# Kernel tuning notes

Measured on AMD Instinct MI355X. Metric: run time of the kernel, lower is better.

## Reference

```python
import jax, jax.numpy as jnp
import numpy as np

B, T = 2, 1024
V, D, H, L = 32000, 1024, 16, 8
DH = D // H  # 64
ROPE_BASE = 1000.0
EPS = 1e-6


def _rms_norm(x):
    # F.rms_norm(x, (C,), eps=1e-6)
    ms = jnp.mean(jnp.square(x), axis=-1, keepdims=True)
    return x * jax.lax.rsqrt(ms + EPS)


def _rope_tables(t_len):
    quarter = DH // 4
    inv_freq = jnp.concatenate([
        ROPE_BASE ** (-jnp.arange(quarter, dtype=jnp.float32) / quarter),
        jnp.zeros(quarter, dtype=jnp.float32),
    ])  # [DH/2]
    theta = jnp.arange(t_len, dtype=jnp.float32)[:, None] * inv_freq[None, :]  # [T, DH/2]
    return jnp.cos(theta), jnp.sin(theta)


def _apply_rope(x, cos, sin):
    # x: [B, H, T, DH]; cos/sin: [T, DH/2] broadcast to [1,1,T,DH/2]
    half = DH // 2
    x1, x2 = x[..., :half], x[..., half:]
    c = cos[None, None]
    s = sin[None, None]
    return jnp.concatenate([c * x1 - s * x2, s * x1 + c * x2], axis=-1).astype(x.dtype)


def setup_inputs() -> dict:
    key = jax.random.key(0)
    ks = jax.random.split(key, 7)
    s = 0.02
    return {
        "x_indices": jax.random.randint(ks[0], (B, T), 0, V, dtype=jnp.int32),
        "embedding": jax.random.normal(ks[1], (V, D), dtype=jnp.float32) * s,
        "Wqkv": jax.random.normal(ks[2], (L, 3 * D, D), dtype=jnp.float32) * s,
        "Wout": jax.random.normal(ks[3], (L, D, D), dtype=jnp.float32) * s,
        "W1": jax.random.normal(ks[4], (L, 4 * D, D), dtype=jnp.float32) * s,
        "W2": jax.random.normal(ks[5], (L, D, 4 * D), dtype=jnp.float32) * s,
        "lm_head": jax.random.normal(ks[6], (V, D), dtype=jnp.float32) * s,
    }


def reference(x_indices, embedding, Wqkv, Wout, W1, W2, lm_head):
    x = embedding[x_indices]  # [B, T, D]
    cos, sin = _rope_tables(T)
    causal = jnp.tril(jnp.ones((T, T), dtype=bool))  # [T, T]
    neg = jnp.finfo(x.dtype).min
    scale = 1.0 / np.sqrt(DH)

    for l in range(L):
        n = _rms_norm(x)
        qkv = jnp.einsum('btd,ed->bte', n, Wqkv[l])  # [B, T, 3D]
        qkv = qkv.reshape(B, T, 3, H, DH)
        q = jnp.transpose(qkv[:, :, 0], (0, 2, 1, 3))  # [B, H, T, DH]
        k = jnp.transpose(qkv[:, :, 1], (0, 2, 1, 3))
        v = jnp.transpose(qkv[:, :, 2], (0, 2, 1, 3))
        q = _apply_rope(q, cos, sin)
        k = _apply_rope(k, cos, sin)
        scores = jnp.einsum('bhqd,bhkd->bhqk', q, k) * scale
        scores = jnp.where(causal[None, None], scores, neg)
        attn = jax.nn.softmax(scores, axis=-1)
        ctx = jnp.einsum('bhqk,bhkd->bhqd', attn, v)
        ctx = jnp.transpose(ctx, (0, 2, 1, 3)).reshape(B, T, D)
        x = x + jnp.einsum('btd,ed->bte', ctx, Wout[l])
        n = _rms_norm(x)
        h = jnp.square(jax.nn.relu(jnp.einsum('btd,fd->btf', n, W1[l])))  # [B, T, 4D]
        x = x + jnp.einsum('btf,df->btd', h, W2[l])

    logits = jnp.einsum('btd,vd->btv', _rms_norm(x), lm_head)
    return logits.astype(jnp.float32)
```

## Files before the change

### kernel.cpp

```cpp
#include <hip/hip_runtime.h>
#include <hip/hip_bf16.h>
#include <cmath>
#include <cstdint>

#define B_  2
#define T_  1024
#define V_  32000
#define D_  1024
#define H_  16
#define L_  8
#define DH_ 64

typedef __attribute__((ext_vector_type(8))) short bf16x8;
typedef __attribute__((ext_vector_type(4))) float f32x4;

__device__ __forceinline__ ushort f2bf(float f) {
    union { float f; uint32_t u; } v; v.f = f;
    uint32_t r = v.u + 0x7FFFu + ((v.u >> 16) & 1u);
    return (ushort)(r >> 16);
}
__device__ __forceinline__ float bf2f(ushort u) {
    union { uint32_t u; float f; } v; v.u = ((uint32_t)u) << 16;
    return v.f;
}

__device__ __forceinline__ void async_copy16(const void* g, void* l) {
    __builtin_amdgcn_global_load_lds(
        (const __attribute__((address_space(1))) void*)g,
        (__attribute__((address_space(3))) void*)l, 16, 0, 0);
}

__global__ __launch_bounds__(256) void k_cast(const float4* __restrict__ in,
                                              ushort4* __restrict__ out, int n4) {
    for (int i = blockIdx.x * 256 + threadIdx.x; i < n4; i += gridDim.x * 256) {
        float4 v = in[i];
        out[i] = make_ushort4(f2bf(v.x), f2bf(v.y), f2bf(v.z), f2bf(v.w));
    }
}

__global__ void k_rope_tables(float* __restrict__ cosT, float* __restrict__ sinT) {
    int t = blockIdx.x;
    int i = threadIdx.x;
    float invf = (i < 16) ? powf(1000.0f, -(float)i / 16.0f) : 0.0f;
    float th = (float)t * invf;
    cosT[t * 32 + i] = cosf(th);
    sinT[t * 32 + i] = sinf(th);
}

__global__ __launch_bounds__(256) void k_gather(const int* __restrict__ idx,
                                                const float* __restrict__ emb,
                                                float* __restrict__ x,
                                                ushort* __restrict__ xb,
                                                float* __restrict__ ss) {
    int row = blockIdx.x;
    int id = idx[row];
    float4 v = ((const float4*)(emb + (size_t)id * D_))[threadIdx.x];
    ((float4*)(x + (size_t)row * D_))[threadIdx.x] = v;
    *(ushort4*)(xb + (size_t)row * D_ + threadIdx.x * 4) =
        make_ushort4(f2bf(v.x), f2bf(v.y), f2bf(v.z), f2bf(v.w));
    float s = v.x * v.x + v.y * v.y + v.z * v.z + v.w * v.w;
    #pragma unroll
    for (int off = 1; off < 64; off <<= 1) s += __shfl_xor(s, off);
    __shared__ float wsum[4];
    int lane = threadIdx.x & 63, wv = threadIdx.x >> 6;
    if (lane == 0) wsum[wv] = s;
    __syncthreads();
    if (threadIdx.x == 0) ss[row] = wsum[0] + wsum[1] + wsum[2] + wsum[3];
}

template<int BN, int EPI, bool OUTBF, bool CONVB, bool RSCALE, bool SSOUT>
__global__ __launch_bounds__(256, 2) void k_mfma_gemm(const ushort* __restrict__ A,
                                                      const void* __restrict__ Wp,
                                                      void* __restrict__ Cp,
                                                      const float* __restrict__ Res,
                                                      const float* __restrict__ cosT,
                                                      const float* __restrict__ sinT,
                                                      const float* __restrict__ ssIn,
                                                      float* __restrict__ ssOut,
                                                      ushort* __restrict__ xbOut,
                                                      int M, int N, int K) {
    constexpr int BM = 128;
    constexpr int MI = 4;
    constexpr int NI = BN / 32;
    constexpr bool DBUF = (BN <= 128);
    constexpr int NB = DBUF ? 2 : 1;
    __shared__ ushort As[NB][BM][64];
    __shared__ ushort Bs[NB][BN][64];
    const int tid = threadIdx.x;
    const int wid = tid >> 6, lane = tid & 63;
    const int wr = wid >> 1, wc = wid & 1;
    const int r16 = lane & 15, kc = lane >> 4;
    const int rx = (r16 & 7) << 4;
    const int srow8 = tid >> 3;
    const int sdcp = tid & 7;

    const int nwg = gridDim.x * gridDim.y;
    int orig = blockIdx.y * gridDim.x + blockIdx.x;
    int swz = (nwg & 7) ? orig : ((orig & 7) * (nwg >> 3) + (orig >> 3));
    const size_t bm = (size_t)(swz % gridDim.x) * BM;
    const size_t bn = (size_t)(swz / gridDim.x) * BN;

    auto stage = [&](int buf, int k0) {
        #pragma unroll
        for (int i = 0; i < 4; i++) {
            const int row = i * 32 + srow8;
            const ushort* g = A + (bm + row) * (size_t)K + k0 + ((sdcp ^ (row & 7)) * 8);
            async_copy16(g, (char*)As + buf * (BM * 128) + (i * 256 + tid) * 16);
        }
        if constexpr (!CONVB) {
            const ushort* Wb = (const ushort*)Wp;
            #pragma unroll
            for (int i = 0; i < BN / 32; i++) {
                const int row = i * 32 + srow8;
                const ushort* g = Wb + (bn + row) * (size_t)K + k0 + ((sdcp ^ (row & 7)) * 8);
                async_copy16(g, (char*)Bs + buf * (BN * 128) + (i * 256 + tid) * 16);
            }
        } else {
            const float* Wf = (const float*)Wp;
            #pragma unroll
            for (int i = 0; i < BN / 32; i++) {
                const int row = i * 32 + srow8;
                const float* src = Wf + (bn + row) * (size_t)K + k0 + sdcp * 8;
                float4 v0 = *(const float4*)(src);
                float4 v1 = *(const float4*)(src + 4);
                union { ushort u[8]; bf16x8 v; } tmp;
                tmp.u[0] = f2bf(v0.x); tmp.u[1] = f2bf(v0.y);
                tmp.u[2] = f2bf(v0.z); tmp.u[3] = f2bf(v0.w);
                tmp.u[4] = f2bf(v1.x); tmp.u[5] = f2bf(v1.y);
                tmp.u[6] = f2bf(v1.z); tmp.u[7] = f2bf(v1.w);
                *(bf16x8*)((char*)Bs + buf * (BN * 128) + row * 128 + ((sdcp ^ (row & 7)) << 4)) = tmp.v;
            }
        }
    };

    f32x4 acc[MI][NI];
    #pragma unroll
    for (int mi = 0; mi < MI; mi++)
        #pragma unroll
        for (int ni = 0; ni < NI; ni++) {
            f32x4 z = {0.f, 0.f, 0.f, 0.f};
            acc[mi][ni] = z;
        }

    auto compute = [&](int buf) {
        #pragma unroll
        for (int kk = 0; kk < 2; kk++) {
            bf16x8 af[MI], bfr[NI];
            #pragma unroll
            for (int mi = 0; mi < MI; mi++)
                af[mi] = *(const bf16x8*)((const char*)As + buf * (BM * 128) +
                                          (wr * 64 + mi * 16 + r16) * 128 +
                                          ((kk * 64 + kc * 16) ^ rx));
            #pragma unroll
            for (int ni = 0; ni < NI; ni++)
                bfr[ni] = *(const bf16x8*)((const char*)Bs + buf * (BN * 128) +
                                           (wc * (BN / 2) + ni * 16 + r16) * 128 +
                                           ((kk * 64 + kc * 16) ^ rx));
            #pragma unroll
            for (int mi = 0; mi < MI; mi++)
                #pragma unroll
                for (int ni = 0; ni < NI; ni++)
                    acc[mi][ni] = __builtin_amdgcn_mfma_f32_16x16x32_bf16(af[mi], bfr[ni],
                                                                          acc[mi][ni], 0, 0, 0);
        }
    };

    const int KSTEPS = K >> 6;
    if constexpr (DBUF) {
        stage(0, 0);
        __syncthreads();
        for (int step = 0; step < KSTEPS; ++step) {
            const int cur = step & 1;
            if (step + 1 < KSTEPS) stage(cur ^ 1, (step + 1) << 6);
            compute(cur);
            __syncthreads();
        }
    } else {
        for (int step = 0; step < KSTEPS; ++step) {
            stage(0, step << 6);
            __syncthreads();
            compute(0);
            __syncthreads();
        }
    }

    #pragma unroll
    for (int mi = 0; mi < MI; mi++) {
        #pragma unroll
        for (int j = 0; j < 4; j++) {
            const size_t row = bm + wr * 64 + mi * 16 + (lane >> 4) * 4 + j;
            if constexpr (RSCALE) {
                const float sc = rsqrtf(ssIn[row] * (1.0f / 1024.0f) + 1e-6f);
                #pragma unroll
                for (int ni = 0; ni < NI; ni++) acc[mi][ni][j] *= sc;
            }
            if constexpr (EPI == 3) {
                static_assert(BN == 128, "rope epilogue assumes BN=128");
                const int sec = (int)((bn + wc * 64) >> 10);
                if (sec < 2) {
                    const int t = (int)(row & (T_ - 1));
                    #pragma unroll
                    for (int np = 0; np < 2; np++) {
                        const int i1 = np * 16 + r16;
                        float c = cosT[t * 32 + i1], s = sinT[t * 32 + i1];
                        float x1 = acc[mi][np][j], x2 = acc[mi][np + 2][j];
                        acc[mi][np][j]     = c * x1 - s * x2;
                        acc[mi][np + 2][j] = s * x1 + c * x2;
                    }
                }
            }
            float ssq = 0.f;
            #pragma unroll
            for (int ni = 0; ni < NI; ni++) {
                const size_t col = bn + wc * (BN / 2) + ni * 16 + r16;
                float v = acc[mi][ni][j];
                if constexpr (EPI == 1) v += Res[row * N + col];
                if constexpr (EPI == 2) { v = fmaxf(v, 0.f); v *= v; }
                if constexpr (SSOUT) {
                    ssq += v * v;
                    xbOut[row * N + col] = f2bf(v);
                }
                if constexpr (OUTBF) {
                    ((ushort*)Cp)[row * N + col] = f2bf(v);
                } else if constexpr (EPI == 0) {
                    __builtin_nontemporal_store(v, (float*)Cp + row * N + col);
                } else {
                    ((float*)Cp)[row * N + col] = v;
                }
            }
            if constexpr (SSOUT) {
                #pragma unroll
                for (int off = 1; off < 16; off <<= 1) ssq += __shfl_xor(ssq, off);
                if (r16 == 0) atomicAdd(&ssOut[row], ssq);
            }
        }
    }
}

__global__ __launch_bounds__(256) void k_attn_pair(const ushort* __restrict__ qkv,
                                                   ushort* __restrict__ ctx) {
    __shared__ __align__(16) char lds[32768];
    const int tid = threadIdx.x;
    const int w = tid >> 6, lane = tid & 63;
    const int r16 = lane & 15, kc = lane >> 4;
    const int rx = (r16 & 7) << 4;
    const int ip = blockIdx.x;
    const int qb[2] = { ip * 64, (15 - ip) * 64 };
    const int bh = blockIdx.y, b = bh >> 4, h = bh & 15;
    const size_t tok0 = (size_t)b * T_;
    const ushort* kg = qkv + tok0 * (3 * D_) + D_ + h * DH_;
    const ushort* vg = qkv + tok0 * (3 * D_) + 2 * D_ + h * DH_;
    const float SCALE_LOG2E = 0.125f * 1.44269504089f;

    #pragma unroll
    for (int t = 0; t < 2; t++) {
        const ushort* qg = qkv + (tok0 + qb[t]) * (3 * D_) + h * DH_;
        #pragma unroll
        for (int i = 0; i < 2; i++) {
            int slot = i * 256 + tid;
            int row = slot >> 3, dcp = slot & 7;
            int d0 = (dcp ^ (row & 7)) * 8;
            async_copy16(qg + (size_t)row * (3 * D_) + d0, lds + 16384 + t * 8192 + slot * 16);
        }
    }
    __syncthreads();
    bf16x8 aq[2][2];
    #pragma unroll
    for (int t = 0; t < 2; t++)
        #pragma unroll
        for (int ks = 0; ks < 2; ks++) {
            int row = w * 16 + r16;
            aq[t][ks] = *(const bf16x8*)(lds + 16384 + t * 8192 + row * 128 +
                                         ((ks * 64 + kc * 16) ^ rx));
        }

    f32x4 o[2][4];
    float m[2][4], l[2][4];
    #pragma unroll
    for (int t = 0; t < 2; t++)
        #pragma unroll
        for (int nd = 0; nd < 4; nd++) {
            f32x4 z = {0.f, 0.f, 0.f, 0.f};
            o[t][nd] = z;
            m[t][nd] = -1e30f; l[t][nd] = 0.f;
        }

    const int nch = 16 - ip;
    for (int ch = 0; ch < nch; ch++) {
        const int kb = ch << 6;
        __syncthreads();
        #pragma unroll
        for (int i = 0; i < 2; i++) {
            int slot = i * 256 + tid;
            int row = slot >> 3, dcp = slot & 7;
            int d0 = (dcp ^ (row & 7)) * 8;
            async_copy16(kg + (size_t)(kb + row) * (3 * D_) + d0, lds + slot * 16);
        }
        {
            int key = tid >> 2, dbase = (tid & 3) * 16;
            const ushort* src = vg + (size_t)(kb + key) * (3 * D_) + dbase;
            bf16x8 v0 = *(const bf16x8*)(src);
            bf16x8 v1 = *(const bf16x8*)(src + 8);
            #pragma unroll
            for (int e = 0; e < 8; e++) {
                int d = dbase + e;
                *(ushort*)(lds + 8192 + d * 128 + ((key * 2) ^ ((d & 7) << 4))) = (ushort)v0[e];
                d = dbase + 8 + e;
                *(ushort*)(lds + 8192 + d * 128 + ((key * 2) ^ ((d & 7) << 4))) = (ushort)v1[e];
            }
        }
        __syncthreads();

        const int nact = (ch <= ip) ? 2 : 1;
        for (int tt = 0; tt < nact; tt++) {
            const int t = (tt == 0) ? 1 : 0;
            const int pq = 16384 + t * 8192;
            f32x4 s[4];
            #pragma unroll
            for (int ni = 0; ni < 4; ni++) { f32x4 z = {0.f, 0.f, 0.f, 0.f}; s[ni] = z; }
            __builtin_amdgcn_s_setprio(1);
            #pragma unroll
            for (int ks = 0; ks < 2; ks++)
                #pragma unroll
                for (int ni = 0; ni < 4; ni++) {
                    int row = ni * 16 + r16;
                    bf16x8 kf = *(const bf16x8*)(lds + row * 128 + ((ks * 64 + kc * 16) ^ rx));
                    s[ni] = __builtin_amdgcn_mfma_f32_16x16x32_bf16(aq[t][ks], kf, s[ni], 0, 0, 0);
                }
            __builtin_amdgcn_s_setprio(0);

            const bool diag = (kb == qb[t]);
            float corr[4];
            #pragma unroll
            for (int j = 0; j < 4; j++) {
                const int qrow = qb[t] + w * 16 + kc * 4 + j;
                #pragma unroll
                for (int ni = 0; ni < 4; ni++) {
                    float v = s[ni][j] * SCALE_LOG2E;
                    if (diag) { int key = kb + ni * 16 + r16; if (key > qrow) v = -1e30f; }
                    s[ni][j] = v;
                }
                float tmax = fmaxf(fmaxf(s[0][j], s[1][j]), fmaxf(s[2][j], s[3][j]));
                #pragma unroll
                for (int off = 1; off < 16; off <<= 1) tmax = fmaxf(tmax, __shfl_xor(tmax, off));
                float mn = fmaxf(m[t][j], tmax);
                corr[j] = exp2f(m[t][j] - mn);
                m[t][j] = mn;
                float ps = 0.f;
                #pragma unroll
                for (int ni = 0; ni < 4; ni++) {
                    float p = exp2f(s[ni][j] - mn);
                    s[ni][j] = p;
                    ps += p;
                }
                #pragma unroll
                for (int off = 1; off < 16; off <<= 1) ps += __shfl_xor(ps, off);
                l[t][j] = l[t][j] * corr[j] + ps;
            }
            #pragma unroll
            for (int ni = 0; ni < 4; ni++)
                #pragma unroll
                for (int j = 0; j < 4; j++) {
                    int row = w * 16 + kc * 4 + j;
                    *(ushort*)(lds + pq + row * 128 + ((ni * 32 + r16 * 2) ^ ((row & 7) << 4))) = f2bf(s[ni][j]);
                }
            #pragma unroll
            for (int nd = 0; nd < 4; nd++)
                #pragma unroll
                for (int j = 0; j < 4; j++) o[t][nd][j] *= corr[j];
            __builtin_amdgcn_s_setprio(1);
            #pragma unroll
            for (int ks = 0; ks < 2; ks++) {
                int prow = w * 16 + r16;
                bf16x8 pf = *(const bf16x8*)(lds + pq + prow * 128 + ((ks * 64 + kc * 16) ^ rx));
                #pragma unroll
                for (int nd = 0; nd < 4; nd++) {
                    int drow = nd * 16 + r16;
                    bf16x8 vf = *(const bf16x8*)(lds + 8192 + drow * 128 + ((ks * 64 + kc * 16) ^ rx));
                    o[t][nd] = __builtin_amdgcn_mfma_f32_16x16x32_bf16(pf, vf, o[t][nd], 0, 0, 0);
                }
            }
            __builtin_amdgcn_s_setprio(0);
        }
    }

    #pragma unroll
    for (int t = 0; t < 2; t++)
        #pragma unroll
        for (int j = 0; j < 4; j++) {
            float inv = 1.0f / l[t][j];
            int row = qb[t] + w * 16 + kc * 4 + j;
            ushort* dst = ctx + (tok0 + row) * D_ + h * DH_;
            #pragma unroll
            for (int nd = 0; nd < 4; nd++)
                dst[nd * 16 + r16] = f2bf(o[t][nd][j] * inv);
        }
}

extern "C" void kernel_launch(void* const* d_in, const int* in_sizes, int n_in,
                              void* d_out, int out_size, void* d_ws, size_t ws_size,
                              hipStream_t stream) {
    const int*   xi   = (const int*)d_in[0];
    const float* emb  = (const float*)d_in[1];
    const float* Wqkv = (const float*)d_in[2];
    const float* Wout = (const float*)d_in[3];
    const float* W1   = (const float*)d_in[4];
    const float* W2   = (const float*)d_in[5];
    const float* lmh  = (const float*)d_in[6];
    float* out = (float*)d_out;

    const size_t NT = (size_t)B_ * T_;
    size_t off = 0;
    auto carve = [&](size_t bytes) -> char* {
        char* r = (char*)d_ws + off;
        off += (bytes + 255) & ~(size_t)255;
        return r;
    };
    float*  xbuf = (float*)carve(NT * D_ * 4);
    ushort* xb   = (ushort*)carve(NT * D_ * 2);
    ushort* qkv  = (ushort*)carve(NT * 3 * D_ * 2);
    ushort* ctxb = (ushort*)carve(NT * D_ * 2);
    ushort* hb   = (ushort*)carve(NT * 4 * D_ * 2);
    float*  cosT = (float*)carve(T_ * 32 * 4);
    float*  sinT = (float*)carve(T_ * 32 * 4);
    float*  ssA  = (float*)carve(17 * NT * 4);
    float*  ss_q = ssA;
    float*  ss_f = ssA + 9 * NT;

    const size_t nWqkv = (size_t)L_ * 3 * D_ * D_;
    const size_t nWout = (size_t)L_ * D_ * D_;
    const size_t nW1   = (size_t)L_ * 4 * D_ * D_;
    const size_t nW2   = (size_t)L_ * 4 * D_ * D_;
    const size_t nLmh  = (size_t)V_ * D_;
    ushort* WqkvB = (ushort*)carve(nWqkv * 2);
    ushort* WoutB = (ushort*)carve(nWout * 2);
    ushort* W1B   = (ushort*)carve(nW1 * 2);
    ushort* W2B   = (ushort*)carve(nW2 * 2);
    ushort* lmhB  = (ushort*)carve(nLmh * 2);
    const bool preconv = (off <= ws_size);

    hipMemsetAsync(ssA, 0, 17 * NT * 4, stream);

    if (preconv) {
        k_cast<<<dim3(2048), dim3(256), 0, stream>>>((const float4*)Wqkv, (ushort4*)WqkvB, (int)(nWqkv / 4));
        k_cast<<<dim3(2048), dim3(256), 0, stream>>>((const float4*)Wout, (ushort4*)WoutB, (int)(nWout / 4));
        k_cast<<<dim3(2048), dim3(256), 0, stream>>>((const float4*)W1,   (ushort4*)W1B,   (int)(nW1 / 4));
        k_cast<<<dim3(2048), dim3(256), 0, stream>>>((const float4*)W2,   (ushort4*)W2B,   (int)(nW2 / 4));
        k_cast<<<dim3(2048), dim3(256), 0, stream>>>((const float4*)lmh,  (ushort4*)lmhB,  (int)(nLmh / 4));
    }

#define LAUNCH_GEMM(BN, EPI, OUTBF, RSC, SSO, GX, GY, Aq, Wb16, Wf32, Cq, Rq, ssin, ssout, xbo, Mv, Nv, Kv) \
    do {                                                                                     \
        if (preconv)                                                                         \
            k_mfma_gemm<BN, EPI, OUTBF, false, RSC, SSO><<<dim3(GX, GY), dim3(256), 0, stream>>>( \
                (const ushort*)(Aq), (const void*)(Wb16), (void*)(Cq), (Rq), cosT, sinT,     \
                (ssin), (ssout), (xbo), Mv, Nv, Kv);                                         \
        else                                                                                 \
            k_mfma_gemm<BN, EPI, OUTBF, true, RSC, SSO><<<dim3(GX, GY), dim3(256), 0, stream>>>( \
                (const ushort*)(Aq), (const void*)(Wf32), (void*)(Cq), (Rq), cosT, sinT,     \
                (ssin), (ssout), (xbo), Mv, Nv, Kv);                                         \
    } while (0)

    k_rope_tables<<<dim3(T_), dim3(32), 0, stream>>>(cosT, sinT);
    k_gather<<<dim3(NT), dim3(256), 0, stream>>>(xi, emb, xbuf, xb, ss_q);

    for (int l = 0; l < L_; l++) {
        LAUNCH_GEMM(128, 3, true, true, false, 16, 24, xb,
                    WqkvB + (size_t)l * 3 * D_ * D_, Wqkv + (size_t)l * 3 * D_ * D_,
                    qkv, nullptr, ss_q + (size_t)l * NT, nullptr, nullptr, (int)NT, 3 * D_, D_);
        k_attn_pair<<<dim3(8, B_ * H_), dim3(256), 0, stream>>>(qkv, ctxb);
        LAUNCH_GEMM(64, 1, false, false, true, 16, 16, ctxb,
                    WoutB + (size_t)l * D_ * D_, Wout + (size_t)l * D_ * D_,
                    xbuf, xbuf, nullptr, ss_f + (size_t)l * NT, xb, (int)NT, D_, D_);
        LAUNCH_GEMM(128, 2, true, true, false, 16, 32, xb,
                    W1B + (size_t)l * 4 * D_ * D_, W1 + (size_t)l * 4 * D_ * D_,
                    hb, nullptr, ss_f + (size_t)l * NT, nullptr, nullptr, (int)NT, 4 * D_, D_);
        LAUNCH_GEMM(64, 1, false, false, true, 16, 16, hb,
                    W2B + (size_t)l * 4 * D_ * D_, W2 + (size_t)l * 4 * D_ * D_,
                    xbuf, xbuf, nullptr, ss_q + (size_t)(l + 1) * NT, xb, (int)NT, D_, 4 * D_);
    }
    LAUNCH_GEMM(256, 0, false, true, false, 16, 125, xb, lmhB, lmh, out, nullptr,
                ss_q + (size_t)L_ * NT, nullptr, nullptr, (int)NT, V_, D_);
#undef LAUNCH_GEMM
}
```

Before: 1.943 ms.

## Replace paired-query attention with single-block attention and double-buffered K/V prefetch

Attention now gives each workgroup one 64-row query block instead of a balanced pair of blocks, so the grid doubles to 16x32 workgroups. K and V tiles are double-buffered in a larger LDS area. The next chunk's K copy and V register load are issued before the current chunk's compute, and one barrier per chunk replaces two. The aim is to hide global load latency and raise parallelism, at the cost of uneven per-block work under the causal mask and more LDS per block.

```diff
diff --git a/kernel.cpp b/kernel.cpp
--- a/kernel.cpp
+++ b/kernel.cpp
@@ -237,164 +237,169 @@
     }
 }
 
-__global__ __launch_bounds__(256) void k_attn_pair(const ushort* __restrict__ qkv,
-                                                   ushort* __restrict__ ctx) {
-    __shared__ __align__(16) char lds[32768];
+__global__ __launch_bounds__(256) void k_attn_sb(const ushort* __restrict__ qkv,
+                                                 ushort* __restrict__ ctx) {
+    __shared__ __align__(16) char lds[40960];
     const int tid = threadIdx.x;
     const int w = tid >> 6, lane = tid & 63;
     const int r16 = lane & 15, kc = lane >> 4;
     const int rx = (r16 & 7) << 4;
-    const int ip = blockIdx.x;
-    const int qb[2] = { ip * 64, (15 - ip) * 64 };
+    const int qb = blockIdx.x * 64;
     const int bh = blockIdx.y, b = bh >> 4, h = bh & 15;
     const size_t tok0 = (size_t)b * T_;
+    const ushort* qg = qkv + (tok0 + qb) * (3 * D_) + h * DH_;
     const ushort* kg = qkv + tok0 * (3 * D_) + D_ + h * DH_;
     const ushort* vg = qkv + tok0 * (3 * D_) + 2 * D_ + h * DH_;
     const float SCALE_LOG2E = 0.125f * 1.44269504089f;
 
-    #pragma unroll
-    for (int t = 0; t < 2; t++) {
-        const ushort* qg = qkv + (tok0 + qb[t]) * (3 * D_) + h * DH_;
-        #pragma unroll
-        for (int i = 0; i < 2; i++) {
-            int slot = i * 256 + tid;
-            int row = slot >> 3, dcp = slot & 7;
-            int d0 = (dcp ^ (row & 7)) * 8;
-            async_copy16(qg + (size_t)row * (3 * D_) + d0, lds + 16384 + t * 8192 + slot * 16);
-        }
-    }
+    const int srow = tid >> 3, sdcp = tid & 7;
+    const int vkey = tid >> 2, vdb = (tid & 3) * 16;
+
+    #pragma unroll
+    for (int i = 0; i < 2; i++) {
+        int slot = i * 256 + tid;
+        int row = slot >> 3, dcp = slot & 7;
+        int d0 = (dcp ^ (row & 7)) * 8;
+        async_copy16(qg + (size_t)row * (3 * D_) + d0, lds + 32768 + slot * 16);
+    }
+    #pragma unroll
+    for (int i = 0; i < 2; i++) {
+        int slot = i * 256 + tid;
+        int row = slot >> 3, dcp = slot & 7;
+        int d0 = (dcp ^ (row & 7)) * 8;
+        async_copy16(kg + (size_t)row * (3 * D_) + d0, lds + slot * 16);
+    }
+    bf16x8 v0 = *(const bf16x8*)(vg + (size_t)vkey * (3 * D_) + vdb);
+    bf16x8 v1 = *(const bf16x8*)(vg + (size_t)vkey * (3 * D_) + vdb + 8);
     __syncthreads();
-    bf16x8 aq[2][2];
-    #pragma unroll
-    for (int t = 0; t < 2; t++)
-        #pragma unroll
-        for (int ks = 0; ks < 2; ks++) {
-            int row = w * 16 + r16;
-            aq[t][ks] = *(const bf16x8*)(lds + 16384 + t * 8192 + row * 128 +
-                                         ((ks * 64 + kc * 16) ^ rx));
-        }
-
-    f32x4 o[2][4];
-    float m[2][4], l[2][4];
-    #pragma unroll
-    for (int t = 0; t < 2; t++)
-        #pragma unroll
-        for (int nd = 0; nd < 4; nd++) {
-            f32x4 z = {0.f, 0.f, 0.f, 0.f};
-            o[t][nd] = z;
-            m[t][nd] = -1e30f; l[t][nd] = 0.f;
-        }
-
-    const int nch = 16 - ip;
+
+    bf16x8 aq[2];
+    #pragma unroll
+    for (int ks = 0; ks < 2; ks++) {
+        int row = w * 16 + r16;
+        aq[ks] = *(const bf16x8*)(lds + 32768 + row * 128 + ((ks * 64 + kc * 16) ^ rx));
+    }
+    #pragma unroll
+    for (int e = 0; e < 8; e++) {
+        int d = vdb + e;
+        *(ushort*)(lds + 8192 + d * 128 + ((vkey * 2) ^ ((d & 7) << 4))) = (ushort)v0[e];
+        d = vdb + 8 + e;
+        *(ushort*)(lds + 8192 + d * 128 + ((vkey * 2) ^ ((d & 7) << 4))) = (ushort)v1[e];
+    }
+    __syncthreads();
+
+    f32x4 o[4];
+    float m[4], l[4], corr[4];
+    #pragma unroll
+    for (int nd = 0; nd < 4; nd++) { f32x4 z = {0.f, 0.f, 0.f, 0.f}; o[nd] = z; }
+    #pragma unroll
+    for (int j = 0; j < 4; j++) { m[j] = -1e30f; l[j] = 0.f; }
+
+    const int nch = blockIdx.x + 1;
     for (int ch = 0; ch < nch; ch++) {
         const int kb = ch << 6;
+        const int cur = (ch & 1) * 16384;
+        const int nxt = ((ch & 1) ^ 1) * 16384;
+        const bool pre = (ch + 1 < nch);
+        if (pre) {
+            #pragma unroll
+            for (int i = 0; i < 2; i++) {
+                int slot = i * 256 + tid;
+                int row = slot >> 3, dcp = slot & 7;
+                int d0 = (dcp ^ (row & 7)) * 8;
+                async_copy16(kg + (size_t)(kb + 64 + row) * (3 * D_) + d0, lds + nxt + slot * 16);
+            }
+            v0 = *(const bf16x8*)(vg + (size_t)(kb + 64 + vkey) * (3 * D_) + vdb);
+            v1 = *(const bf16x8*)(vg + (size_t)(kb + 64 + vkey) * (3 * D_) + vdb + 8);
+        }
+
+        f32x4 s[4];
+        #pragma unroll
+        for (int ni = 0; ni < 4; ni++) { f32x4 z = {0.f, 0.f, 0.f, 0.f}; s[ni] = z; }
+        __builtin_amdgcn_s_setprio(1);
+        #pragma unroll
+        for (int ks = 0; ks < 2; ks++)
+            #pragma unroll
+            for (int ni = 0; ni < 4; ni++) {
+                int row = ni * 16 + r16;
+                bf16x8 kf = *(const bf16x8*)(lds + cur + row * 128 + ((ks * 64 + kc * 16) ^ rx));
+                s[ni] = __builtin_amdgcn_mfma_f32_16x16x32_bf16(aq[ks], kf, s[ni], 0, 0, 0);
+            }
+        __builtin_amdgcn_s_setprio(0);
+
+        const bool diag = (kb == qb);
+        #pragma unroll
+        for (int j = 0; j < 4; j++) {
+            const int qrow = qb + w * 16 + kc * 4 + j;
+            #pragma unroll
+            for (int ni = 0; ni < 4; ni++) {
+                float v = s[ni][j] * SCALE_LOG2E;
+                if (diag) { int key = kb + ni * 16 + r16; if (key > qrow) v = -1e30f; }
+                s[ni][j] = v;
+            }
+            float tmax = fmaxf(fmaxf(s[0][j], s[1][j]), fmaxf(s[2][j], s[3][j]));
+            #pragma unroll
+            for (int off = 1; off < 16; off <<= 1) tmax = fmaxf(tmax, __shfl_xor(tmax, off));
+            float mn = fmaxf(m[j], tmax);
+            corr[j] = exp2f(m[j] - mn);
+            m[j] = mn;
+            float ps = 0.f;
+            #pragma unroll
+            for (int ni = 0; ni < 4; ni++) {
+                float p = exp2f(s[ni][j] - mn);
+                s[ni][j] = p;
+                ps += p;
+            }
+            #pragma unroll
+            for (int off = 1; off < 16; off <<= 1) ps += __shfl_xor(ps, off);
+            l[j] = l[j] * corr[j] + ps;
+        }
+        #pragma unroll
+        for (int ni = 0; ni < 4; ni++)
+            #pragma unroll
+            for (int j = 0; j < 4; j++) {
+                int row = w * 16 + kc * 4 + j;
+                *(ushort*)(lds + 32768 + row * 128 + ((ni * 32 + r16 * 2) ^ ((row & 7) << 4))) = f2bf(s[ni][j]);
+            }
+        #pragma unroll
+        for (int nd = 0; nd < 4; nd++)
+            #pragma unroll
+            for (int j = 0; j < 4; j++) o[nd][j] *= corr[j];
+        __builtin_amdgcn_s_setprio(1);
+        #pragma unroll
+        for (int ks = 0; ks < 2; ks++) {
+            int prow = w * 16 + r16;
+            bf16x8 pf = *(const bf16x8*)(lds + 32768 + prow * 128 + ((ks * 64 + kc * 16) ^ rx));
+            #pragma unroll
+            for (int nd = 0; nd < 4; nd++) {
+                int drow = nd * 16 + r16;
+                bf16x8 vf = *(const bf16x8*)(lds + cur + 8192 + drow * 128 + ((ks * 64 + kc * 16) ^ rx));
+                o[nd] = __builtin_amdgcn_mfma_f32_16x16x32_bf16(pf, vf, o[nd], 0, 0, 0);
+            }
+        }
+        __builtin_amdgcn_s_setprio(0);
+
+        if (pre) {
+            #pragma unroll
+            for (int e = 0; e < 8; e++) {
+                int d = vdb + e;
+                *(ushort*)(lds + nxt + 8192 + d * 128 + ((vkey * 2) ^ ((d & 7) << 4))) = (ushort)v0[e];
+                d = vdb + 8 + e;
+                *(ushort*)(lds + nxt + 8192 + d * 128 + ((vkey * 2) ^ ((d & 7) << 4))) = (ushort)v1[e];
+            }
+        }
         __syncthreads();
-        #pragma unroll
-        for (int i = 0; i < 2; i++) {
-            int slot = i * 256 + tid;
-            int row = slot >> 3, dcp = slot & 7;
-            int d0 = (dcp ^ (row & 7)) * 8;
-            async_copy16(kg + (size_t)(kb + row) * (3 * D_) + d0, lds + slot * 16);
-        }
-        {
-            int key = tid >> 2, dbase = (tid & 3) * 16;
-            const ushort* src = vg + (size_t)(kb + key) * (3 * D_) + dbase;
-            bf16x8 v0 = *(const bf16x8*)(src);
-            bf16x8 v1 = *(const bf16x8*)(src + 8);
-            #pragma unroll
-            for (int e = 0; e < 8; e++) {
-                int d = dbase + e;
-                *(ushort*)(lds + 8192 + d * 128 + ((key * 2) ^ ((d & 7) << 4))) = (ushort)v0[e];
-                d = dbase + 8 + e;
-                *(ushort*)(lds + 8192 + d * 128 + ((key * 2) ^ ((d & 7) << 4))) = (ushort)v1[e];
-            }
-        }
-        __syncthreads();
-
-        const int nact = (ch <= ip) ? 2 : 1;
-        for (int tt = 0; tt < nact; tt++) {
-            const int t = (tt == 0) ? 1 : 0;
-            const int pq = 16384 + t * 8192;
-            f32x4 s[4];
-            #pragma unroll
-            for (int ni = 0; ni < 4; ni++) { f32x4 z = {0.f, 0.f, 0.f, 0.f}; s[ni] = z; }
-            __builtin_amdgcn_s_setprio(1);
-            #pragma unroll
-            for (int ks = 0; ks < 2; ks++)
-                #pragma unroll
-                for (int ni = 0; ni < 4; ni++) {
-                    int row = ni * 16 + r16;
-                    bf16x8 kf = *(const bf16x8*)(lds + row * 128 + ((ks * 64 + kc * 16) ^ rx));
-                    s[ni] = __builtin_amdgcn_mfma_f32_16x16x32_bf16(aq[t][ks], kf, s[ni], 0, 0, 0);
-                }
-            __builtin_amdgcn_s_setprio(0);
-
-            const bool diag = (kb == qb[t]);
-            float corr[4];
-            #pragma unroll
-            for (int j = 0; j < 4; j++) {
-                const int qrow = qb[t] + w * 16 + kc * 4 + j;
-                #pragma unroll
-                for (int ni = 0; ni < 4; ni++) {
-                    float v = s[ni][j] * SCALE_LOG2E;
-                    if (diag) { int key = kb + ni * 16 + r16; if (key > qrow) v = -1e30f; }
-                    s[ni][j] = v;
-                }
-                float tmax = fmaxf(fmaxf(s[0][j], s[1][j]), fmaxf(s[2][j], s[3][j]));
-                #pragma unroll
-                for (int off = 1; off < 16; off <<= 1) tmax = fmaxf(tmax, __shfl_xor(tmax, off));
-                float mn = fmaxf(m[t][j], tmax);
-                corr[j] = exp2f(m[t][j] - mn);
-                m[t][j] = mn;
-                float ps = 0.f;
-                #pragma unroll
-                for (int ni = 0; ni < 4; ni++) {
-                    float p = exp2f(s[ni][j] - mn);
-                    s[ni][j] = p;
-                    ps += p;
-                }
-                #pragma unroll
-                for (int off = 1; off < 16; off <<= 1) ps += __shfl_xor(ps, off);
-                l[t][j] = l[t][j] * corr[j] + ps;
-            }
-            #pragma unroll
-            for (int ni = 0; ni < 4; ni++)
-                #pragma unroll
-                for (int j = 0; j < 4; j++) {
-                    int row = w * 16 + kc * 4 + j;
-                    *(ushort*)(lds + pq + row * 128 + ((ni * 32 + r16 * 2) ^ ((row & 7) << 4))) = f2bf(s[ni][j]);
-                }
-            #pragma unroll
-            for (int nd = 0; nd < 4; nd++)
-                #pragma unroll
-                for (int j = 0; j < 4; j++) o[t][nd][j] *= corr[j];
-            __builtin_amdgcn_s_setprio(1);
-            #pragma unroll
-            for (int ks = 0; ks < 2; ks++) {
-                int prow = w * 16 + r16;
-                bf16x8 pf = *(const bf16x8*)(lds + pq + prow * 128 + ((ks * 64 + kc * 16) ^ rx));
-                #pragma unroll
-                for (int nd = 0; nd < 4; nd++) {
-                    int drow = nd * 16 + r16;
-                    bf16x8 vf = *(const bf16x8*)(lds + 8192 + drow * 128 + ((ks * 64 + kc * 16) ^ rx));
-                    o[t][nd] = __builtin_amdgcn_mfma_f32_16x16x32_bf16(pf, vf, o[t][nd], 0, 0, 0);
-                }
-            }
-            __builtin_amdgcn_s_setprio(0);
-        }
-    }
-
-    #pragma unroll
-    for (int t = 0; t < 2; t++)
-        #pragma unroll
-        for (int j = 0; j < 4; j++) {
-            float inv = 1.0f / l[t][j];
-            int row = qb[t] + w * 16 + kc * 4 + j;
-            ushort* dst = ctx + (tok0 + row) * D_ + h * DH_;
-            #pragma unroll
-            for (int nd = 0; nd < 4; nd++)
-                dst[nd * 16 + r16] = f2bf(o[t][nd][j] * inv);
-        }
+    }
+
+    #pragma unroll
+    for (int j = 0; j < 4; j++) {
+        float inv = 1.0f / l[j];
+        int row = qb + w * 16 + kc * 4 + j;
+        ushort* dst = ctx + (tok0 + row) * D_ + h * DH_;
+        #pragma unroll
+        for (int nd = 0; nd < 4; nd++)
+            dst[nd * 16 + r16] = f2bf(o[nd][j] * inv);
+    }
 }
 
 extern "C" void kernel_launch(void* const* d_in, const int* in_sizes, int n_in,
@@ -468,7 +473,7 @@
         LAUNCH_GEMM(128, 3, true, true, false, 16, 24, xb,
                     WqkvB + (size_t)l * 3 * D_ * D_, Wqkv + (size_t)l * 3 * D_ * D_,
                     qkv, nullptr, ss_q + (size_t)l * NT, nullptr, nullptr, (int)NT, 3 * D_, D_);
-        k_attn_pair<<<dim3(8, B_ * H_), dim3(256), 0, stream>>>(qkv, ctxb);
+        k_attn_sb<<<dim3(16, B_ * H_), dim3(256), 0, stream>>>(qkv, ctxb);
         LAUNCH_GEMM(64, 1, false, false, true, 16, 16, ctxb,
                     WoutB + (size_t)l * D_ * D_, Wout + (size_t)l * D_ * D_,
                     xbuf, xbuf, nullptr, ss_f + (size_t)l * NT, xb, (int)NT, D_, D_);
```

After: 1.975 ms. No clear change (+1.7%).
